# Kernel tuning notes

Measured on AMD Instinct MI355X. Metric: run time of the kernel, lower is better.

The kernel has to match this reference:

```python
import jax, jax.numpy as jnp
import numpy as np

N, E, H, C, HID = 50000, 800000, 4, 24, 96
NUM_ZONES, BATCH = 6, 64
NEG_SLOPE = 0.2


def _ln(x, scale, bias, eps=1e-5):
    m = jnp.mean(x, -1, keepdims=True)
    v = jnp.var(x, -1, keepdims=True)
    return (x - m) * jax.lax.rsqrt(v + eps) * scale + bias


def _gat_layer(x, src, dst, edge_attr, W, a_src, a_dst, We, a_edge, bias):
    # add self-loops (PyG default, fill_value='mean' -> per-dst mean of edge_attr)
    deg = jax.ops.segment_sum(jnp.ones((E,), x.dtype), dst, num_segments=N)
    loop_attr = jax.ops.segment_sum(edge_attr, dst, num_segments=N) / jnp.clip(deg, 1.0)[:, None]
    loops = jnp.arange(N, dtype=src.dtype)
    s = jnp.concatenate([src, loops])
    d = jnp.concatenate([dst, loops])
    ea = jnp.concatenate([edge_attr, loop_attr], axis=0)  # [E+N, edge_dim]

    h = (x @ W).reshape(N, H, C)                      # shared lin_src/lin_dst
    e = (ea @ We).reshape(-1, H, C)                   # edge feature projection
    a_s = jnp.einsum('nhc,hc->nh', h, a_src)
    a_d = jnp.einsum('nhc,hc->nh', h, a_dst)
    alpha = a_s[s] + a_d[d] + jnp.einsum('ehc,hc->eh', e, a_edge)  # [E+N, H]
    alpha = jnp.where(alpha > 0, alpha, NEG_SLOPE * alpha)

    # segment softmax over incoming edges of each dst node
    mx = jax.ops.segment_max(alpha, d, num_segments=N)
    ex = jnp.exp(alpha - mx[d])
    den = jax.ops.segment_sum(ex, d, num_segments=N)
    attn = ex / (den[d] + 1e-16)                      # [E+N, H]

    msg = attn[:, :, None] * h[s]                     # [E+N, H, C]
    out = jax.ops.segment_sum(msg, d, num_segments=N).reshape(N, H * C)
    return out + bias


def setup_inputs() -> dict:
    key = jax.random.key(0)
    ks = jax.random.split(key, 40)
    p = {}
    p['x'] = jax.random.normal(ks[0], (N, 12), jnp.float32)
    p['edge_index'] = jax.random.randint(ks[1], (2, E), 0, N)
    p['edge_attr'] = jax.random.normal(ks[2], (E, 4), jnp.float32)
    p['zone_idx'] = jax.random.randint(ks[3], (BATCH * NUM_ZONES,), 0, N)
    g = lambda k, s: jax.random.normal(k, s, jnp.float32) * 0.1
    p['in_w1'] = g(ks[4], (12, HID)); p['in_b1'] = jnp.zeros((HID,))
    p['in_w2'] = g(ks[5], (HID, HID)); p['in_b2'] = jnp.zeros((HID,))
    p['conv_w'] = g(ks[6], (4, HID, HID))
    p['conv_att_src'] = g(ks[7], (4, H, C))
    p['conv_att_dst'] = g(ks[8], (4, H, C))
    p['conv_lin_edge'] = g(ks[9], (4, 4, HID))
    p['conv_att_edge'] = g(ks[10], (4, H, C))
    p['conv_bias'] = jnp.zeros((4, HID))
    p['norm_scale'] = jnp.ones((4, HID)); p['norm_bias'] = jnp.zeros((4, HID))
    for i, (name, o) in enumerate([('cong', 2), ('delay', 1), ('jit', 1)]):
        p[f'{name}_w1'] = g(ks[11 + 6 * i], (HID, HID)); p[f'{name}_b1'] = jnp.zeros((HID,))
        p[f'{name}_w2'] = g(ks[12 + 6 * i], (HID, HID // 2)); p[f'{name}_b2'] = jnp.zeros((HID // 2,))
        p[f'{name}_w3'] = g(ks[13 + 6 * i], (HID // 2, o)); p[f'{name}_b3'] = jnp.zeros((o,))
    return p


def _head(z, w1, b1, w2, b2, w3, b3):
    z = jax.nn.relu(z @ w1 + b1)
    z = jax.nn.relu(z @ w2 + b2)
    return z @ w3 + b3


def reference(x, edge_index, edge_attr, zone_idx,
              in_w1, in_b1, in_w2, in_b2,
              conv_w, conv_att_src, conv_att_dst, conv_lin_edge, conv_att_edge, conv_bias,
              norm_scale, norm_bias,
              cong_w1, cong_b1, cong_w2, cong_b2, cong_w3, cong_b3,
              delay_w1, delay_b1, delay_w2, delay_b2, delay_w3, delay_b3,
              jit_w1, jit_b1, jit_w2, jit_b2, jit_w3, jit_b3):
    src, dst = edge_index[0], edge_index[1]
    h = jax.nn.relu(x @ in_w1 + in_b1) @ in_w2 + in_b2
    for i in range(4):
        res = h
        h = _gat_layer(h, src, dst, edge_attr, conv_w[i], conv_att_src[i],
                       conv_att_dst[i], conv_lin_edge[i], conv_att_edge[i], conv_bias[i])
        h = jax.nn.elu(h)
        h = _ln(h + res, norm_scale[i], norm_bias[i])
        # dropout: eval mode -> identity
    z = h[zone_idx]                                   # [BATCH*NUM_ZONES, HID]
    preds = jnp.concatenate([
        _head(z, cong_w1, cong_b1, cong_w2, cong_b2, cong_w3, cong_b3),
        _head(z, delay_w1, delay_b1, delay_w2, delay_b2, delay_w3, delay_b3),
        _head(z, jit_w1, jit_b1, jit_w2, jit_b2, jit_w3, jit_b3)], axis=-1)
    return preds.reshape(BATCH, NUM_ZONES, 4)
```

## Files before the change

### kernel.cpp

```cpp
#include <hip/hip_runtime.h>
#include <hip/hip_fp16.h>

#define NN 50000
#define EE 800000
#define HIDD 96
#define NZ 384

typedef __attribute__((ext_vector_type(8))) _Float16 half8;
typedef __attribute__((ext_vector_type(4))) float floatx4;

struct __align__(16) Rec{ int src; int pad; float4 ea; };

__global__ void k_deg(const int* __restrict__ dst, int* __restrict__ deg){
  int e=blockIdx.x*blockDim.x+threadIdx.x;
  if(e>=EE) return;
  atomicAdd(&deg[dst[e]],1);
}

__global__ void k_scan1(const int* __restrict__ deg, int* __restrict__ off, int* __restrict__ part){
  __shared__ int sd[256];
  int t=threadIdx.x, b=blockIdx.x;
  int base=b*1024+t*4;
  int v0=(base+0<NN)?deg[base+0]:0;
  int v1=(base+1<NN)?deg[base+1]:0;
  int v2=(base+2<NN)?deg[base+2]:0;
  int v3=(base+3<NN)?deg[base+3]:0;
  int s=v0+v1+v2+v3;
  sd[t]=s; __syncthreads();
  for(int o=1;o<256;o<<=1){
    int x=(t>=o)?sd[t-o]:0;
    __syncthreads();
    sd[t]+=x;
    __syncthreads();
  }
  int ep=sd[t]-s;
  if(base+0<NN) off[base+0]=ep;
  if(base+1<NN) off[base+1]=ep+v0;
  if(base+2<NN) off[base+2]=ep+v0+v1;
  if(base+3<NN) off[base+3]=ep+v0+v1+v2;
  if(t==255) part[b]=sd[255];
}

__global__ void k_scan2(int* part, int* off, int nb){
  if(threadIdx.x==0&&blockIdx.x==0){
    int run=0;
    for(int i=0;i<nb;i++){ int x=part[i]; part[i]=run; run+=x; }
    off[NN]=run;
  }
}

__global__ void k_scan3(const int* __restrict__ part, int* __restrict__ off, int* __restrict__ cur){
  int i=blockIdx.x*blockDim.x+threadIdx.x;
  if(i<NN){ int v=off[i]+part[i>>10]; off[i]=v; cur[i]=v; }
}

__global__ void k_scatter(const int* __restrict__ src, const int* __restrict__ dst,
                          const float* __restrict__ eattr, int* __restrict__ cur,
                          Rec* __restrict__ rec){
  int e=blockIdx.x*blockDim.x+threadIdx.x;
  if(e>=EE) return;
  int d=dst[e];
  int p=atomicAdd(&cur[d],1);
  Rec r; r.src=src[e]; r.pad=0; r.ea=*(const float4*)(eattr+(size_t)e*4);
  rec[p]=r;
}

__global__ void k_prepw(const float* __restrict__ conv_w, const float* __restrict__ a_src,
                        const float* __restrict__ a_dst, const float* __restrict__ lin_e,
                        const float* __restrict__ a_e,
                        float* __restrict__ Watt, float* __restrict__ Mm){
  int t=blockIdx.x*blockDim.x+threadIdx.x;
  const int WT=4*96*8;
  if(t<WT){
    int l=t/(96*8); int rem=t-l*(96*8); int k=rem>>3; int j=rem&7;
    int hh=j&3;
    const float* W=conv_w+(size_t)l*96*96+(size_t)k*96;
    const float* a=((j>=4)?a_dst:a_src)+l*96+hh*24;
    float v=0.f;
    #pragma unroll
    for(int c=0;c<24;c++) v+=W[hh*24+c]*a[c];
    Watt[t]=v;
  } else if(t<WT+64){
    int q=t-WT; int l=q>>4; int i=(q>>2)&3; int hh=q&3;
    const float* We=lin_e+(size_t)l*4*96+(size_t)i*96;
    const float* a=a_e+l*96+hh*24;
    float v=0.f;
    #pragma unroll
    for(int c=0;c<24;c++) v+=We[hh*24+c]*a[c];
    Mm[q]=v;
  }
}

__global__ void k_mlp1(const float* __restrict__ x, const float* __restrict__ w,
                       const float* __restrict__ b, float* __restrict__ out){
  int i=blockIdx.x*blockDim.x+threadIdx.x;
  if(i>=NN) return;
  float xv[12];
  #pragma unroll
  for(int k=0;k<12;k++) xv[k]=x[(size_t)i*12+k];
  for(int j=0;j<HIDD;j++){
    float a=b[j];
    #pragma unroll
    for(int k=0;k<12;k++) a+=xv[k]*w[k*HIDD+j];
    out[(size_t)i*HIDD+j]=fmaxf(a,0.f);
  }
}

__global__ __launch_bounds__(256) void k_gemm96(const float* __restrict__ A,
                                                const float* __restrict__ W,
                                                const float* __restrict__ bias,
                                                float* __restrict__ C){
  __shared__ float As[64][100];
  __shared__ float Ws[96][96];
  int t=threadIdx.x;
  int r0=blockIdx.x*64;
  for(int i=t;i<96*96/4;i+=256) ((float4*)&Ws[0][0])[i]=((const float4*)W)[i];
  for(int i=t;i<64*24;i+=256){
    int rr=i/24, cc=(i-rr*24)*4; int g=r0+rr;
    float4 v = (g<NN)? *(const float4*)(A+(size_t)g*96+cc) : float4{0.f,0.f,0.f,0.f};
    *(float4*)&As[rr][cc]=v;
  }
  __syncthreads();
  int cg=t&15, rg=t>>4;
  int c0=cg*6, r=rg*4;
  float acc[4][6];
  #pragma unroll
  for(int i=0;i<4;i++)
    #pragma unroll
    for(int j=0;j<6;j++) acc[i][j]=0.f;
  for(int k4=0;k4<96;k4+=4){
    float4 a0=*(float4*)&As[r  ][k4];
    float4 a1=*(float4*)&As[r+1][k4];
    float4 a2=*(float4*)&As[r+2][k4];
    float4 a3=*(float4*)&As[r+3][k4];
    #pragma unroll
    for(int kk=0;kk<4;kk++){
      float2 w01=*(float2*)&Ws[k4+kk][c0];
      float2 w23=*(float2*)&Ws[k4+kk][c0+2];
      float2 w45=*(float2*)&Ws[k4+kk][c0+4];
      float wv[6]={w01.x,w01.y,w23.x,w23.y,w45.x,w45.y};
      float av0=((float*)&a0)[kk],av1=((float*)&a1)[kk],av2=((float*)&a2)[kk],av3=((float*)&a3)[kk];
      #pragma unroll
      for(int j=0;j<6;j++){
        acc[0][j]+=av0*wv[j];
        acc[1][j]+=av1*wv[j];
        acc[2][j]+=av2*wv[j];
        acc[3][j]+=av3*wv[j];
      }
    }
  }
  #pragma unroll
  for(int i=0;i<4;i++){
    int g=r0+r+i;
    if(g<NN){
      #pragma unroll
      for(int j=0;j<6;j++) C[(size_t)g*96+c0+j]=acc[i][j]+bias[c0+j];
    }
  }
}

__global__ __launch_bounds__(256) void k_gemmM(const float* __restrict__ A,
    const float* __restrict__ W, const float* __restrict__ Watt8,
    __half* __restrict__ hp16, float* __restrict__ att){
  __shared__ half8 Bl[3][7][64];
  int t=threadIdx.x;
  for(int i=t;i<3*7*64;i+=256){
    int kk=i/448; int rem=i-kk*448; int nb=rem>>6; int l=rem&63;
    int kbase=kk*32+((l>>4)<<3);
    int n=nb*16+(l&15);
    half8 v;
    #pragma unroll
    for(int j=0;j<8;j++){
      int k=kbase+j;
      float x=(n<96)?W[k*96+n]:((n<104)?Watt8[k*8+(n-96)]:0.f);
      v[j]=(_Float16)x;
    }
    Bl[kk][nb][l]=v;
  }
  __syncthreads();
  int wid=t>>6, l=t&63;
  int row0=blockIdx.x*64+wid*16;
  int arow=row0+(l&15);
  bool rv=arow<NN;
  const float* Ar=A+(size_t)(rv?arow:0)*96;
  half8 a[3];
  #pragma unroll
  for(int kk=0;kk<3;kk++){
    int kb=kk*32+((l>>4)<<3);
    floatx4 lo=*(const floatx4*)(Ar+kb);
    floatx4 hi=*(const floatx4*)(Ar+kb+4);
    half8 v;
    #pragma unroll
    for(int j=0;j<4;j++){ v[j]=(_Float16)(rv?lo[j]:0.f); v[j+4]=(_Float16)(rv?hi[j]:0.f); }
    a[kk]=v;
  }
  int col16=l&15;
  int rbase=row0+((l>>4)<<2);
  #pragma unroll
  for(int nb=0;nb<7;nb++){
    floatx4 acc={0.f,0.f,0.f,0.f};
    #pragma unroll
    for(int kk=0;kk<3;kk++)
      acc=__builtin_amdgcn_mfma_f32_16x16x32_f16(a[kk],Bl[kk][nb][l],acc,0,0,0);
    int col=nb*16+col16;
    if(col<96){
      #pragma unroll
      for(int r=0;r<4;r++){
        int g=rbase+r;
        if(g<NN) hp16[(size_t)g*96+col]=__float2half(acc[r]);
      }
    } else if(col<104){
      #pragma unroll
      for(int r=0;r<4;r++){
        int g=rbase+r;
        if(g<NN) att[(size_t)g*8+(col-96)]=acc[r];
      }
    }
  }
}

__global__ __launch_bounds__(256) void k_agg(const __half* __restrict__ hp16,
    const float* __restrict__ att, float* __restrict__ h,
    const int* __restrict__ off, const Rec* __restrict__ rec,
    const float* __restrict__ Mm, const float* __restrict__ bias,
    const float* __restrict__ nsc, const float* __restrict__ nbi){
  __shared__ float w4[16][17][4];
  __shared__ int   roA[16][17];
  int tid=threadIdx.x;
  int sg=tid>>4, sl=tid&15;
  int n=blockIdx.x*16+sg;
  if(n>=NN) return;
  float M[16];
  #pragma unroll
  for(int i=0;i<16;i++) M[i]=Mm[i];
  const float4 ad=*(const float4*)(att+(size_t)n*8+4);
  int b0=off[n], deg=off[n+1]-b0;
  float invdeg=1.f/(float)(deg>0?deg:1);
  int hL=sl>>2;
  int sloff=sl*12;
  float ds0=0.f,ds1=0.f,ds2=0.f,ds3=0.f;
  float sx=0.f,sy=0.f,sz=0.f,sw=0.f;
  float acc[6]={0.f,0.f,0.f,0.f,0.f,0.f};
  const char* hb=(const char*)hp16;

  for(int cs=0;cs<deg;cs+=16){
    int idx=cs+sl;
    bool valid=idx<deg;
    float w0=0.f,w1=0.f,w2=0.f,w3=0.f; int ro=0;
    if(valid){
      int ei=b0+idx;
      int s=rec[ei].src;
      float4 ea=rec[ei].ea;
      ro=s*192;
      sx+=ea.x; sy+=ea.y; sz+=ea.z; sw+=ea.w;
      const float4 as=*(const float4*)(att+(size_t)s*8);
      float a0=as.x+ad.x+ea.x*M[0]+ea.y*M[4]+ea.z*M[8] +ea.w*M[12];
      float a1=as.y+ad.y+ea.x*M[1]+ea.y*M[5]+ea.z*M[9] +ea.w*M[13];
      float a2=as.z+ad.z+ea.x*M[2]+ea.y*M[6]+ea.z*M[10]+ea.w*M[14];
      float a3=as.w+ad.w+ea.x*M[3]+ea.y*M[7]+ea.z*M[11]+ea.w*M[15];
      a0=a0>0.f?a0:0.2f*a0; a1=a1>0.f?a1:0.2f*a1;
      a2=a2>0.f?a2:0.2f*a2; a3=a3>0.f?a3:0.2f*a3;
      w0=__expf(a0); w1=__expf(a1); w2=__expf(a2); w3=__expf(a3);
      ds0+=w0; ds1+=w1; ds2+=w2; ds3+=w3;
    }
    *(float4*)&w4[sg][sl][0]=float4{w0,w1,w2,w3};
    roA[sg][sl]=ro;
    int nc=deg-cs; if(nc>16) nc=16;
    if(nc>0){
      float ev0=w4[sg][0][hL];
      uint3 u0=*(const uint3*)(hb+(size_t)(unsigned)roA[sg][0]+sloff);
      for(int j=1;j<nc;j++){
        float ev1=w4[sg][j][hL];
        uint3 u1=*(const uint3*)(hb+(size_t)(unsigned)roA[sg][j]+sloff);
        float2 f0=__half22float2(*(__half2*)&u0.x);
        float2 f1=__half22float2(*(__half2*)&u0.y);
        float2 f2=__half22float2(*(__half2*)&u0.z);
        acc[0]+=ev0*f0.x; acc[1]+=ev0*f0.y;
        acc[2]+=ev0*f1.x; acc[3]+=ev0*f1.y;
        acc[4]+=ev0*f2.x; acc[5]+=ev0*f2.y;
        ev0=ev1; u0=u1;
      }
      float2 f0=__half22float2(*(__half2*)&u0.x);
      float2 f1=__half22float2(*(__half2*)&u0.y);
      float2 f2=__half22float2(*(__half2*)&u0.z);
      acc[0]+=ev0*f0.x; acc[1]+=ev0*f0.y;
      acc[2]+=ev0*f1.x; acc[3]+=ev0*f1.y;
      acc[4]+=ev0*f2.x; acc[5]+=ev0*f2.y;
    }
  }
  #pragma unroll
  for(int m=1;m<16;m<<=1){
    ds0+=__shfl_xor(ds0,m); ds1+=__shfl_xor(ds1,m);
    ds2+=__shfl_xor(ds2,m); ds3+=__shfl_xor(ds3,m);
    sx +=__shfl_xor(sx ,m); sy +=__shfl_xor(sy ,m);
    sz +=__shfl_xor(sz ,m); sw +=__shfl_xor(sw ,m);
  }
  float lx=sx*invdeg, ly=sy*invdeg, lz=sz*invdeg, lw=sw*invdeg;
  const float4 aself=*(const float4*)(att+(size_t)n*8);
  float b0a=aself.x+ad.x+lx*M[0]+ly*M[4]+lz*M[8] +lw*M[12];
  float b1a=aself.y+ad.y+lx*M[1]+ly*M[5]+lz*M[9] +lw*M[13];
  float b2a=aself.z+ad.z+lx*M[2]+ly*M[6]+lz*M[10]+lw*M[14];
  float b3a=aself.w+ad.w+lx*M[3]+ly*M[7]+lz*M[11]+lw*M[15];
  b0a=b0a>0.f?b0a:0.2f*b0a; b1a=b1a>0.f?b1a:0.2f*b1a;
  b2a=b2a>0.f?b2a:0.2f*b2a; b3a=b3a>0.f?b3a:0.2f*b3a;
  float e0=__expf(b0a),e1=__expf(b1a),e2=__expf(b2a),e3=__expf(b3a);
  ds0+=e0; ds1+=e1; ds2+=e2; ds3+=e3;
  float eL=(hL==0)?e0:((hL==1)?e1:((hL==2)?e2:e3));
  {
    const char* rp=hb+(size_t)n*192+sloff;
    uint3 u=*(const uint3*)rp;
    float2 f0=__half22float2(*(__half2*)&u.x);
    float2 f1=__half22float2(*(__half2*)&u.y);
    float2 f2=__half22float2(*(__half2*)&u.z);
    acc[0]+=eL*f0.x; acc[1]+=eL*f0.y;
    acc[2]+=eL*f1.x; acc[3]+=eL*f1.y;
    acc[4]+=eL*f2.x; acc[5]+=eL*f2.y;
  }
  float dL=(hL==0)?ds0:((hL==1)?ds1:((hL==2)?ds2:ds3));
  float rinv=1.f/(dL+1e-16f);
  const float* hrow=h+(size_t)n*HIDD+(size_t)sl*6;
  float2 r01=*(const float2*)(hrow);
  float2 r23=*(const float2*)(hrow+2);
  float2 r45=*(const float2*)(hrow+4);
  float rr[6]={r01.x,r01.y,r23.x,r23.y,r45.x,r45.y};
  const float* bp=bias+sl*6;
  float t[6];
  #pragma unroll
  for(int c=0;c<6;c++){
    float v=acc[c]*rinv+bp[c];
    v=v>0.f?v:expm1f(v);
    t[c]=v+rr[c];
  }
  float s1l=t[0]+t[1]+t[2]+t[3]+t[4]+t[5];
  float s2l=t[0]*t[0]+t[1]*t[1]+t[2]*t[2]+t[3]*t[3]+t[4]*t[4]+t[5]*t[5];
  #pragma unroll
  for(int m=1;m<16;m<<=1){ s1l+=__shfl_xor(s1l,m); s2l+=__shfl_xor(s2l,m); }
  float mean=s1l*(1.f/96.f);
  float var=s2l*(1.f/96.f)-mean*mean;
  float rs=rsqrtf(var+1e-5f);
  float* op=h+(size_t)n*HIDD+(size_t)sl*6;
  const float* sc=nsc+sl*6;
  const float* bi=nbi+sl*6;
  float o[6];
  #pragma unroll
  for(int c=0;c<6;c++) o[c]=(t[c]-mean)*rs*sc[c]+bi[c];
  *(float2*)(op)  =float2{o[0],o[1]};
  *(float2*)(op+2)=float2{o[2],o[3]};
  *(float2*)(op+4)=float2{o[4],o[5]};
}

__global__ __launch_bounds__(256) void k_hd1(const float* __restrict__ h, const int* __restrict__ zone,
    const float* __restrict__ cw1,const float* __restrict__ cb1,
    const float* __restrict__ dw1,const float* __restrict__ db1,
    const float* __restrict__ jw1,const float* __restrict__ jb1,
    float* __restrict__ t1){
  int idx=blockIdx.x*256+threadIdx.x;
  if(idx>=3*NZ*96) return;
  int hd=idx/(NZ*96); int rem=idx-hd*(NZ*96); int row=rem/96; int j=rem-row*96;
  const float* w1=(hd==0)?cw1:((hd==1)?dw1:jw1);
  const float* b1=(hd==0)?cb1:((hd==1)?db1:jb1);
  int n=zone[row];
  const float* hr=h+(size_t)n*96;
  float acc=b1[j];
  #pragma unroll
  for(int k4=0;k4<24;k4++){
    float4 hv=*(const float4*)(hr+k4*4);
    acc+=hv.x*w1[(k4*4+0)*96+j];
    acc+=hv.y*w1[(k4*4+1)*96+j];
    acc+=hv.z*w1[(k4*4+2)*96+j];
    acc+=hv.w*w1[(k4*4+3)*96+j];
  }
  t1[idx]=fmaxf(acc,0.f);
}

__global__ __launch_bounds__(256) void k_hd2(const float* __restrict__ t1,
    const float* __restrict__ cw2,const float* __restrict__ cb2,
    const float* __restrict__ dw2,const float* __restrict__ db2,
    const float* __restrict__ jw2,const float* __restrict__ jb2,
    float* __restrict__ t2){
  int idx=blockIdx.x*256+threadIdx.x;
  if(idx>=3*NZ*48) return;
  int hd=idx/(NZ*48); int rem=idx-hd*(NZ*48); int row=rem/48; int c=rem-row*48;
  const float* w2=(hd==0)?cw2:((hd==1)?dw2:jw2);
  const float* b2=(hd==0)?cb2:((hd==1)?db2:jb2);
  const float* t1r=t1+(size_t)hd*NZ*96+(size_t)row*96;
  float acc=b2[c];
  #pragma unroll
  for(int k4=0;k4<24;k4++){
    float4 tv=*(const float4*)(t1r+k4*4);
    acc+=tv.x*w2[(k4*4+0)*48+c];
    acc+=tv.y*w2[(k4*4+1)*48+c];
    acc+=tv.z*w2[(k4*4+2)*48+c];
    acc+=tv.w*w2[(k4*4+3)*48+c];
  }
  t2[idx]=fmaxf(acc,0.f);
}

__global__ __launch_bounds__(256) void k_hd3(const float* __restrict__ t2,
    const float* __restrict__ cw3,const float* __restrict__ cb3,
    const float* __restrict__ dw3,const float* __restrict__ db3,
    const float* __restrict__ jw3,const float* __restrict__ jb3,
    float* __restrict__ out){
  int idx=blockIdx.x*256+threadIdx.x;
  if(idx>=NZ*4) return;
  int row=idx>>2, o=idx&3;
  int hd=(o<2)?0:((o==2)?1:2);
  int c=(o<2)?o:0;
  int osz=(hd==0)?2:1;
  const float* w3=(hd==0)?cw3:((hd==1)?dw3:jw3);
  const float* b3=(hd==0)?cb3:((hd==1)?db3:jb3);
  const float* t2r=t2+(size_t)hd*NZ*48+(size_t)row*48;
  float acc=b3[c];
  #pragma unroll
  for(int k=0;k<48;k++) acc+=t2r[k]*w3[k*osz+c];
  out[idx]=acc;
}

extern "C" void kernel_launch(void* const* d_in, const int* in_sizes, int n_in,
                              void* d_out, int out_size, void* d_ws, size_t ws_size,
                              hipStream_t stream){
  const float* x       =(const float*)d_in[0];
  const int*   eidx    =(const int*)  d_in[1];
  const float* eattr   =(const float*)d_in[2];
  const int*   zone    =(const int*)  d_in[3];
  const float* in_w1   =(const float*)d_in[4];
  const float* in_b1   =(const float*)d_in[5];
  const float* in_w2   =(const float*)d_in[6];
  const float* in_b2   =(const float*)d_in[7];
  const float* conv_w  =(const float*)d_in[8];
  const float* att_src =(const float*)d_in[9];
  const float* att_dst =(const float*)d_in[10];
  const float* lin_edge=(const float*)d_in[11];
  const float* att_edge=(const float*)d_in[12];
  const float* conv_bias=(const float*)d_in[13];
  const float* nsc     =(const float*)d_in[14];
  const float* nbi     =(const float*)d_in[15];
  float* out=(float*)d_out;

  char* p=(char*)d_ws;
  auto carve=[&](size_t bytes)->char*{ char* r=p; p+=(bytes+255)&~(size_t)255; return r; };
  float*  h    =(float*)carve((size_t)NN*96*4);
  char*   uni  =carve((size_t)NN*96*4);
  float*  hid1 =(float*)uni;
  __half* hp16 =(__half*)uni;
  float*  att  =(float*)(uni+(size_t)NN*96*2);
  Rec*    rec  =(Rec*)  carve((size_t)EE*32);
  int*    deg  =(int*)  carve((size_t)NN*4);
  int*    off  =(int*)  carve((size_t)(NN+1)*4);
  int*    cur  =(int*)  carve((size_t)NN*4);
  float*  Watt =(float*)carve((size_t)4*96*8*4);
  float*  Mm   =(float*)carve(64*4);
  int*    part =(int*)  carve(64*4);
  float*  t1b  =(float*)carve((size_t)3*NZ*96*4);
  float*  t2b  =(float*)carve((size_t)3*NZ*48*4);

  const int* srcp=eidx;
  const int* dstp=eidx+EE;

  hipMemsetAsync(deg,0,(size_t)NN*4,stream);
  k_deg<<<EE/256,256,0,stream>>>(dstp,deg);
  k_scan1<<<49,256,0,stream>>>(deg,off,part);
  k_scan2<<<1,64,0,stream>>>(part,off,49);
  k_scan3<<<(NN+255)/256,256,0,stream>>>(part,off,cur);
  k_scatter<<<EE/256,256,0,stream>>>(srcp,dstp,eattr,cur,rec);
  k_prepw<<<(4*96*8+64+255)/256,256,0,stream>>>(conv_w,att_src,att_dst,lin_edge,att_edge,Watt,Mm);

  k_mlp1<<<(NN+255)/256,256,0,stream>>>(x,in_w1,in_b1,hid1);
  k_gemm96<<<(NN+63)/64,256,0,stream>>>(hid1,in_w2,in_b2,h);

  for(int l=0;l<4;l++){
    k_gemmM<<<(NN+63)/64,256,0,stream>>>(h,conv_w+(size_t)l*96*96,Watt+(size_t)l*96*8,hp16,att);
    k_agg<<<(NN+15)/16,256,0,stream>>>(hp16,att,h,off,rec,Mm+l*16,
                                       conv_bias+l*96,nsc+l*96,nbi+l*96);
  }

  k_hd1<<<(3*NZ*96+255)/256,256,0,stream>>>(h,zone,
    (const float*)d_in[16],(const float*)d_in[17],
    (const float*)d_in[22],(const float*)d_in[23],
    (const float*)d_in[28],(const float*)d_in[29], t1b);
  k_hd2<<<(3*NZ*48+255)/256,256,0,stream>>>(t1b,
    (const float*)d_in[18],(const float*)d_in[19],
    (const float*)d_in[24],(const float*)d_in[25],
    (const float*)d_in[30],(const float*)d_in[31], t2b);
  k_hd3<<<(NZ*4+255)/256,256,0,stream>>>(t2b,
    (const float*)d_in[20],(const float*)d_in[21],
    (const float*)d_in[26],(const float*)d_in[27],
    (const float*)d_in[32],(const float*)d_in[33], out);
}
```

Before: 371.7 us.

## Pack edge records to fp16 attrs and fuse input MLP into first GEMM

Edge records shrink from 32 to 16 bytes by storing the four edge attributes as fp16, which halves the record traffic in the scatter and in the four aggregation passes. The first input-MLP layer (12->96, ReLU) is computed inside the 96x96 GEMM kernel straight into shared memory, so the hidden activation no longer makes a round trip through global memory and one launch goes away. The fp16 edge attributes cost some precision in the attention logits and in the self-loop mean.

```diff
diff --git a/kernel.cpp b/kernel.cpp
--- a/kernel.cpp
+++ b/kernel.cpp
@@ -9,7 +9,7 @@
 typedef __attribute__((ext_vector_type(8))) _Float16 half8;
 typedef __attribute__((ext_vector_type(4))) float floatx4;
 
-struct __align__(16) Rec{ int src; int pad; float4 ea; };
+struct __align__(16) Rec{ int src; __half2 e01; __half2 e23; int pad; };
 
 __global__ void k_deg(const int* __restrict__ dst, int* __restrict__ deg){
   int e=blockIdx.x*blockDim.x+threadIdx.x;
@@ -61,7 +61,11 @@
   if(e>=EE) return;
   int d=dst[e];
   int p=atomicAdd(&cur[d],1);
-  Rec r; r.src=src[e]; r.pad=0; r.ea=*(const float4*)(eattr+(size_t)e*4);
+  float4 ea=*(const float4*)(eattr+(size_t)e*4);
+  Rec r; r.src=src[e];
+  r.e01=__floats2half2_rn(ea.x,ea.y);
+  r.e23=__floats2half2_rn(ea.z,ea.w);
+  r.pad=0;
   rec[p]=r;
 }
 
@@ -91,35 +95,47 @@
   }
 }
 
-__global__ void k_mlp1(const float* __restrict__ x, const float* __restrict__ w,
-                       const float* __restrict__ b, float* __restrict__ out){
-  int i=blockIdx.x*blockDim.x+threadIdx.x;
-  if(i>=NN) return;
-  float xv[12];
-  #pragma unroll
-  for(int k=0;k<12;k++) xv[k]=x[(size_t)i*12+k];
-  for(int j=0;j<HIDD;j++){
-    float a=b[j];
-    #pragma unroll
-    for(int k=0;k<12;k++) a+=xv[k]*w[k*HIDD+j];
-    out[(size_t)i*HIDD+j]=fmaxf(a,0.f);
-  }
-}
-
-__global__ __launch_bounds__(256) void k_gemm96(const float* __restrict__ A,
+__global__ __launch_bounds__(256) void k_gemm96(const float* __restrict__ x,
+                                                const float* __restrict__ w1,
+                                                const float* __restrict__ b1,
                                                 const float* __restrict__ W,
                                                 const float* __restrict__ bias,
                                                 float* __restrict__ C){
   __shared__ float As[64][100];
   __shared__ float Ws[96][96];
+  __shared__ float b1s[96];
   int t=threadIdx.x;
   int r0=blockIdx.x*64;
+  for(int i=t;i<12*96/4;i+=256) ((float4*)&Ws[0][0])[i]=((const float4*)w1)[i];
+  if(t<96) b1s[t]=b1[t];
+  __syncthreads();
+  {
+    int r=t>>2, cq=t&3;
+    int g=r0+r;
+    float xv[12];
+    if(g<NN){
+      float4 v0=*(const float4*)(x+(size_t)g*12);
+      float4 v1=*(const float4*)(x+(size_t)g*12+4);
+      float4 v2=*(const float4*)(x+(size_t)g*12+8);
+      xv[0]=v0.x;xv[1]=v0.y;xv[2]=v0.z;xv[3]=v0.w;
+      xv[4]=v1.x;xv[5]=v1.y;xv[6]=v1.z;xv[7]=v1.w;
+      xv[8]=v2.x;xv[9]=v2.y;xv[10]=v2.z;xv[11]=v2.w;
+    }else{
+      #pragma unroll
+      for(int k=0;k<12;k++) xv[k]=0.f;
+    }
+    const float* w1f=&Ws[0][0];
+    #pragma unroll
+    for(int j=0;j<24;j++){
+      int c=cq+4*j;
+      float a=b1s[c];
+      #pragma unroll
+      for(int k=0;k<12;k++) a+=xv[k]*w1f[k*96+c];
+      As[r][c]=fmaxf(a,0.f);
+    }
+  }
+  __syncthreads();
   for(int i=t;i<96*96/4;i+=256) ((float4*)&Ws[0][0])[i]=((const float4*)W)[i];
-  for(int i=t;i<64*24;i+=256){
-    int rr=i/24, cc=(i-rr*24)*4; int g=r0+rr;
-    float4 v = (g<NN)? *(const float4*)(A+(size_t)g*96+cc) : float4{0.f,0.f,0.f,0.f};
-    *(float4*)&As[rr][cc]=v;
-  }
   __syncthreads();
   int cg=t&15, rg=t>>4;
   int c0=cg*6, r=rg*4;
@@ -249,15 +265,17 @@
     float w0=0.f,w1=0.f,w2=0.f,w3=0.f; int ro=0;
     if(valid){
       int ei=b0+idx;
-      int s=rec[ei].src;
-      float4 ea=rec[ei].ea;
+      Rec rr=rec[ei];
+      int s=rr.src;
+      float2 e01=__half22float2(rr.e01);
+      float2 e23=__half22float2(rr.e23);
       ro=s*192;
-      sx+=ea.x; sy+=ea.y; sz+=ea.z; sw+=ea.w;
+      sx+=e01.x; sy+=e01.y; sz+=e23.x; sw+=e23.y;
       const float4 as=*(const float4*)(att+(size_t)s*8);
-      float a0=as.x+ad.x+ea.x*M[0]+ea.y*M[4]+ea.z*M[8] +ea.w*M[12];
-      float a1=as.y+ad.y+ea.x*M[1]+ea.y*M[5]+ea.z*M[9] +ea.w*M[13];
-      float a2=as.z+ad.z+ea.x*M[2]+ea.y*M[6]+ea.z*M[10]+ea.w*M[14];
-      float a3=as.w+ad.w+ea.x*M[3]+ea.y*M[7]+ea.z*M[11]+ea.w*M[15];
+      float a0=as.x+ad.x+e01.x*M[0]+e01.y*M[4]+e23.x*M[8] +e23.y*M[12];
+      float a1=as.y+ad.y+e01.x*M[1]+e01.y*M[5]+e23.x*M[9] +e23.y*M[13];
+      float a2=as.z+ad.z+e01.x*M[2]+e01.y*M[6]+e23.x*M[10]+e23.y*M[14];
+      float a3=as.w+ad.w+e01.x*M[3]+e01.y*M[7]+e23.x*M[11]+e23.y*M[15];
       a0=a0>0.f?a0:0.2f*a0; a1=a1>0.f?a1:0.2f*a1;
       a2=a2>0.f?a2:0.2f*a2; a3=a3>0.f?a3:0.2f*a3;
       w0=__expf(a0); w1=__expf(a1); w2=__expf(a2); w3=__expf(a3);
@@ -441,10 +459,9 @@
   auto carve=[&](size_t bytes)->char*{ char* r=p; p+=(bytes+255)&~(size_t)255; return r; };
   float*  h    =(float*)carve((size_t)NN*96*4);
   char*   uni  =carve((size_t)NN*96*4);
-  float*  hid1 =(float*)uni;
   __half* hp16 =(__half*)uni;
   float*  att  =(float*)(uni+(size_t)NN*96*2);
-  Rec*    rec  =(Rec*)  carve((size_t)EE*32);
+  Rec*    rec  =(Rec*)  carve((size_t)EE*16);
   int*    deg  =(int*)  carve((size_t)NN*4);
   int*    off  =(int*)  carve((size_t)(NN+1)*4);
   int*    cur  =(int*)  carve((size_t)NN*4);
@@ -465,8 +482,7 @@
   k_scatter<<<EE/256,256,0,stream>>>(srcp,dstp,eattr,cur,rec);
   k_prepw<<<(4*96*8+64+255)/256,256,0,stream>>>(conv_w,att_src,att_dst,lin_edge,att_edge,Watt,Mm);
 
-  k_mlp1<<<(NN+255)/256,256,0,stream>>>(x,in_w1,in_b1,hid1);
-  k_gemm96<<<(NN+63)/64,256,0,stream>>>(hid1,in_w2,in_b2,h);
+  k_gemm96<<<(NN+63)/64,256,0,stream>>>(x,in_w1,in_b1,in_w2,in_b2,h);
 
   for(int l=0;l<4;l++){
     k_gemmM<<<(NN+63)/64,256,0,stream>>>(h,conv_w+(size_t)l*96*96,Watt+(size_t)l*96*8,hp16,att);
```

After: 356.2 us. -4.1%, faster.
